# Kernel optimization log

Measured on AMD Instinct MI355X. Metric: run time of the kernel, lower is better.

## Reference

```python
import jax, jax.numpy as jnp
import numpy as np

CHUNK = 64
EMA_DECAY = 0.99


def setup_inputs() -> dict:
    key = jax.random.key(0)
    ks = jax.random.split(key, 4)
    Bsz, S, H, P, N = 2, 4096, 16, 64, 128
    X = jax.random.normal(ks[0], (Bsz, S, H, P), jnp.float32)
    # negative log-decay rates, as in Mamba-2 (A = -softplus(...) style)
    A = -jnp.abs(jax.random.normal(ks[1], (Bsz, S, H), jnp.float32)) * 0.1
    Bm = jax.random.normal(ks[2], (Bsz, S, H, N), jnp.float32) / np.sqrt(N)
    Cm = jax.random.normal(ks[3], (Bsz, S, H, N), jnp.float32) / np.sqrt(N)
    # ChunkedSurpriseGate parameters / buffers
    log2_alpha_base = jnp.full((H,), -0.15, jnp.float32)
    log2_beta = jnp.zeros((H,), jnp.float32)
    surprise_ema = jnp.ones((H,), jnp.float32)
    return {"X": X, "A": A, "Bm": Bm, "Cm": Cm,
            "log2_alpha_base": log2_alpha_base, "log2_beta": log2_beta,
            "surprise_ema": surprise_ema}


def _chunked_surprise_ssd(X, A, Bm, Cm, log2_alpha_base, log2_beta, surprise_ema):
    Bsz, S, H, P = X.shape
    N = Bm.shape[-1]
    cs = CHUNK
    nC = S // cs  # seqlen chosen divisible by chunk_size (no padding branch)

    # [B, nC, cs, H, ...] -> chunk-major [nC, B, H, cs, ...] for lax.scan
    Xc = X.reshape(Bsz, nC, cs, H, P).transpose(1, 0, 3, 2, 4)   # [nC,B,H,cs,P]
    Ac = A.reshape(Bsz, nC, cs, H).transpose(1, 0, 3, 2)          # [nC,B,H,cs]
    Bc = Bm.reshape(Bsz, nC, cs, H, N).transpose(1, 0, 3, 2, 4)   # [nC,B,H,cs,N]
    Cc = Cm.reshape(Bsz, nC, cs, H, N).transpose(1, 0, 3, 2, 4)   # [nC,B,H,cs,N]

    idx = jnp.arange(cs)
    tri = idx[:, None] >= idx[None, :]  # causal mask for decay matrix L

    # gate constants (per-head)
    alpha_base = 1.0 - jnp.exp2(jnp.clip(log2_alpha_base, -3.32, -0.015))  # [H]
    beta = jnp.exp2(jnp.clip(log2_beta, -2.0, 2.0))                         # [H]

    def step(carry, xs):
        h_prev, h_before, decay_prev, ema = carry
        c, X_c, A_c, B_c, C_c = xs
        first = c == 0

        # --- delayed state-based surprise: ||h_prev - decay_prev * h_before||^2
        err = jnp.mean((h_prev - decay_prev[..., None, None] * h_before) ** 2,
                       axis=(-2, -1))  # [B,H]
        # EMA update (training=True path; torch does it under no_grad)
        ema_new = jax.lax.stop_gradient(EMA_DECAY * ema + (1.0 - EMA_DECAY) * jnp.mean(err, axis=0))
        normalized = err / (ema_new[None, :] + 1e-6)                # [B,H]
        boost = jax.nn.relu(jnp.tanh(beta[None, :] * normalized))
        alpha = jnp.clip(alpha_base[None, :] + (1.0 - alpha_base[None, :]) * boost,
                         0.01, 0.999)
        # torch: decay_scale = (1-alpha).mean().item()  -> detached scalar
        ds = jax.lax.stop_gradient(jnp.mean(1.0 - alpha))
        decay_scale = jnp.where(first, jnp.float32(1.0), ds)
        ema_out = jnp.where(first, ema, ema_new)  # no gate call on chunk 0

        # --- single-chunk SSD ---
        Acs = jnp.cumsum(A_c * decay_scale, axis=-1)                 # [B,H,cs]
        # causal decay matrix L[i,j] = exp(Acs[i]-Acs[j]) for i>=j
        L = jnp.where(tri, jnp.exp(Acs[..., :, None] - Acs[..., None, :]), 0.0)
        CB = jnp.einsum('bhin,bhjn->bhij', C_c, B_c)
        Y_intra = jnp.einsum('bhij,bhjd->bhid', L * CB, X_c)
        decay_from_start = jnp.exp(Acs)                               # [B,H,cs]
        Y_inter = jnp.einsum('bhin,bhnd,bhi->bhid', C_c, h_prev, decay_from_start)
        decay_to_end = jnp.exp(Acs[..., -1:] - Acs)                   # [B,H,cs]
        h_contrib = jnp.einsum('bhtn,bhtd,bht->bhnd', B_c, X_c, decay_to_end)
        decay_total = jnp.exp(Acs[..., -1])                           # [B,H]
        h_end = decay_total[..., None, None] * h_prev + h_contrib

        return (h_end, h_prev, decay_total, ema_out), Y_intra + Y_inter

    h0 = jnp.zeros((Bsz, H, N, P), X.dtype)
    carry0 = (h0, h0, jnp.ones((Bsz, H), X.dtype), surprise_ema)
    xs = (jnp.arange(nC), Xc, Ac, Bc, Cc)
    _, Ys = jax.lax.scan(step, carry0, xs)  # [nC,B,H,cs,P]

    # stack dim=2, permute(0,2,3,1,4), reshape -> [B,S,H,P]
    Y = Ys.transpose(1, 0, 3, 2, 4).reshape(Bsz, S, H, P)
    return Y


def reference(X, A, Bm, Cm, log2_alpha_base, log2_beta, surprise_ema):
    return _chunked_surprise_ssd(X, A, Bm, Cm, log2_alpha_base, log2_beta, surprise_ema)
```

## Files before the change

### kernel.cpp

```cpp
#include <hip/hip_runtime.h>
#include <math.h>


#define CSZ 64
#define NCH 64
#define NHD 16
#define PD  64
#define ND  128
#define BHN 32
#define NTILES 2048
#define GGRID 64
#define SEQ 4096

#define WS_S   0
#define WS_EG  131072
#define WS_DS  262144
#define WS_HC  262400

using bf16x8 = __attribute__((ext_vector_type(8))) short;
using f32x4  = __attribute__((ext_vector_type(4))) float;

__device__ __forceinline__ short f2bf(float f) {
  union { float f; unsigned u; } v; v.f = f;
  unsigned r = (v.u + 0x7FFFu + ((v.u >> 16) & 1u)) >> 16;
  return (short)r;
}

__device__ __forceinline__ float bf2f(short s) {
  union { float f; unsigned u; } v;
  v.u = ((unsigned)(unsigned short)s) << 16;
  return v.f;
}

__device__ __forceinline__ void split4(float4 v, short4& hi, short4& lo) {
  hi.x = f2bf(v.x); lo.x = f2bf(v.x - bf2f(hi.x));
  hi.y = f2bf(v.y); lo.y = f2bf(v.y - bf2f(hi.y));
  hi.z = f2bf(v.z); lo.z = f2bf(v.z - bf2f(hi.z));
  hi.w = f2bf(v.w); lo.w = f2bf(v.w - bf2f(hi.w));
}

__global__ __launch_bounds__(256) void k_gramerr(
    const float* __restrict__ X, const float* __restrict__ A,
    const float* __restrict__ Bm, float* __restrict__ ws)
{
  __shared__ __align__(16) short BhiS[64*72];
  __shared__ __align__(16) short BloS[64*72];
  __shared__ __align__(16) short XhiS[64*72];
  __shared__ __align__(16) short XloS[64*72];
  __shared__ float Sl[CSZ];
  __shared__ float Zl[CSZ];
  short* Mhi = BhiS;
  short* Mlo = BloS;
  short* Uhi = XhiS;
  short* Ulo = XloS;

  const int tile = blockIdx.x;
  const int c  = tile & 63;
  const int bh = tile >> 6;
  const int b = bh >> 4, h = bh & 15;
  const int tid = threadIdx.x;

  const float* Bbase = Bm + ((size_t)(b*SEQ + c*CSZ)*NHD + h)*ND;
  const float* Xbase = X  + ((size_t)(b*SEQ + c*CSZ)*NHD + h)*PD;

  if (tid < CSZ) {
    float v = A[(size_t)(b*SEQ + c*CSZ + tid)*NHD + h];
    #pragma unroll
    for (int d = 1; d < 64; d <<= 1) {
      float n = __shfl_up(v, d);
      if (tid >= d) v += n;
    }
    Sl[tid] = v;
    ws[WS_S + tile*CSZ + tid] = v;
  }

  #pragma unroll
  for (int qq = 0; qq < 4; ++qq) {
    int lin = qq*256 + tid;
    int t = lin >> 4, c4 = (lin & 15)*4;
    float4 v = *(const float4*)(Bbase + (size_t)t*(NHD*ND) + c4);
    short4 hi, lo; split4(v, hi, lo);
    *(short4*)&BhiS[t*72 + c4] = hi;
    *(short4*)&BloS[t*72 + c4] = lo;
  }
  #pragma unroll
  for (int qq = 0; qq < 4; ++qq) {
    int lin = qq*256 + tid;
    int t = lin >> 4, p4 = (lin & 15)*4;
    float4 v = *(const float4*)(Xbase + (size_t)t*(NHD*PD) + p4);
    short4 hi, lo; split4(v, hi, lo);
    *(short4*)&XhiS[t*72 + p4] = hi;
    *(short4*)&XloS[t*72 + p4] = lo;
  }
  __syncthreads();

  if (tid < CSZ) Zl[tid] = Sl[63] - Sl[tid];

  const int w = tid >> 6;
  const int lane = tid & 63;
  const int m = lane & 15, q = lane >> 4;

  f32x4 z4 = {0.f,0.f,0.f,0.f};
  f32x4 gb[4], gx[4];
  #pragma unroll
  for (int i = 0; i < 4; ++i) { gb[i] = z4; gx[i] = z4; }

  #pragma unroll
  for (int kk = 0; kk < 2; ++kk) {
    const int ao = (w*16+m)*72 + kk*32 + q*8;
    bf16x8 ah = *(bf16x8*)&BhiS[ao];
    bf16x8 al = *(bf16x8*)&BloS[ao];
    #pragma unroll
    for (int ct = 0; ct < 4; ++ct) {
      const int bo = (ct*16+m)*72 + kk*32 + q*8;
      bf16x8 bhv = *(bf16x8*)&BhiS[bo];
      bf16x8 blv = *(bf16x8*)&BloS[bo];
      gb[ct] = __builtin_amdgcn_mfma_f32_16x16x32_bf16(ah, bhv, gb[ct], 0,0,0);
      gb[ct] = __builtin_amdgcn_mfma_f32_16x16x32_bf16(ah, blv, gb[ct], 0,0,0);
      gb[ct] = __builtin_amdgcn_mfma_f32_16x16x32_bf16(al, bhv, gb[ct], 0,0,0);
    }
  }
  __syncthreads();

  #pragma unroll
  for (int qq = 0; qq < 4; ++qq) {
    int lin = qq*256 + tid;
    int t = lin >> 4, c4 = (lin & 15)*4;
    float4 v = *(const float4*)(Bbase + (size_t)t*(NHD*ND) + 64 + c4);
    short4 hi, lo; split4(v, hi, lo);
    *(short4*)&BhiS[t*72 + c4] = hi;
    *(short4*)&BloS[t*72 + c4] = lo;
  }
  __syncthreads();

  #pragma unroll
  for (int kk = 0; kk < 2; ++kk) {
    const int ao = (w*16+m)*72 + kk*32 + q*8;
    bf16x8 ah = *(bf16x8*)&BhiS[ao];
    bf16x8 al = *(bf16x8*)&BloS[ao];
    #pragma unroll
    for (int ct = 0; ct < 4; ++ct) {
      const int bo = (ct*16+m)*72 + kk*32 + q*8;
      bf16x8 bhv = *(bf16x8*)&BhiS[bo];
      bf16x8 blv = *(bf16x8*)&BloS[bo];
      gb[ct] = __builtin_amdgcn_mfma_f32_16x16x32_bf16(ah, bhv, gb[ct], 0,0,0);
      gb[ct] = __builtin_amdgcn_mfma_f32_16x16x32_bf16(ah, blv, gb[ct], 0,0,0);
      gb[ct] = __builtin_amdgcn_mfma_f32_16x16x32_bf16(al, bhv, gb[ct], 0,0,0);
    }
  }
  #pragma unroll
  for (int kk = 0; kk < 2; ++kk) {
    const int ao = (w*16+m)*72 + kk*32 + q*8;
    bf16x8 ah = *(bf16x8*)&XhiS[ao];
    bf16x8 al = *(bf16x8*)&XloS[ao];
    #pragma unroll
    for (int ct = 0; ct < 4; ++ct) {
      const int bo = (ct*16+m)*72 + kk*32 + q*8;
      bf16x8 bhv = *(bf16x8*)&XhiS[bo];
      bf16x8 blv = *(bf16x8*)&XloS[bo];
      gx[ct] = __builtin_amdgcn_mfma_f32_16x16x32_bf16(ah, bhv, gx[ct], 0,0,0);
      gx[ct] = __builtin_amdgcn_mfma_f32_16x16x32_bf16(ah, blv, gx[ct], 0,0,0);
      gx[ct] = __builtin_amdgcn_mfma_f32_16x16x32_bf16(al, bhv, gx[ct], 0,0,0);
    }
  }
  __syncthreads();

  #pragma unroll
  for (int ct = 0; ct < 4; ++ct)
    #pragma unroll
    for (int r = 0; r < 4; ++r) {
      int i = w*16 + q*4 + r;
      int j = ct*16 + m;
      float mvf = gb[ct][r]*gx[ct][r]*(1.0f/8192.0f);
      short mh = f2bf(mvf);
      Mhi[i*72 + j] = mh;
      Mlo[i*72 + j] = f2bf(mvf - bf2f(mh));
    }
  #pragma unroll
  for (int qq = 0; qq < 16; ++qq) {
    int idx = qq*256 + tid;
    int g = idx >> 6, t = idx & 63;
    float u = expf(((float)g*(1.0f/63.0f))*Zl[t]);
    short uh = f2bf(u);
    Uhi[g*72 + t] = uh;
    Ulo[g*72 + t] = f2bf(u - bf2f(uh));
  }
  __syncthreads();

  f32x4 wv4[4];
  #pragma unroll
  for (int i = 0; i < 4; ++i) wv4[i] = z4;
  #pragma unroll
  for (int kk = 0; kk < 2; ++kk) {
    const int ao = (w*16+m)*72 + kk*32 + q*8;
    bf16x8 uh = *(bf16x8*)&Uhi[ao];
    bf16x8 ul = *(bf16x8*)&Ulo[ao];
    #pragma unroll
    for (int ct = 0; ct < 4; ++ct) {
      const int bo = (ct*16+m)*72 + kk*32 + q*8;
      bf16x8 mh = *(bf16x8*)&Mhi[bo];
      bf16x8 ml = *(bf16x8*)&Mlo[bo];
      wv4[ct] = __builtin_amdgcn_mfma_f32_16x16x32_bf16(uh, mh, wv4[ct], 0,0,0);
      wv4[ct] = __builtin_amdgcn_mfma_f32_16x16x32_bf16(uh, ml, wv4[ct], 0,0,0);
      wv4[ct] = __builtin_amdgcn_mfma_f32_16x16x32_bf16(ul, mh, wv4[ct], 0,0,0);
    }
  }

  #pragma unroll
  for (int r = 0; r < 4; ++r) {
    int g = w*16 + q*4 + r;
    float e = 0.f;
    #pragma unroll
    for (int ct = 0; ct < 4; ++ct) {
      int t = ct*16 + m;
      float uval = bf2f(Uhi[g*72 + t]) + bf2f(Ulo[g*72 + t]);
      e += wv4[ct][r] * uval;
    }
    e += __shfl_xor(e, 1);
    e += __shfl_xor(e, 2);
    e += __shfl_xor(e, 4);
    e += __shfl_xor(e, 8);
    if (m == 0) ws[WS_EG + (c*GGRID + g)*BHN + bh] = e;
  }
}

__global__ __launch_bounds__(64) void k_gate(
    const float* __restrict__ l2ab, const float* __restrict__ l2b,
    const float* __restrict__ sema, float* __restrict__ ws)
{
  __shared__ __align__(16) float ring[8*GGRID*BHN];
  const int lane = threadIdx.x;
  const int h = lane & 15;
  const float* EG = ws + WS_EG;

  float ab = 0.f, bt = 1.f, ema = 0.f;
  if (lane < NHD) {
    float la = fminf(fmaxf(l2ab[lane], -3.32f), -0.015f);
    ab = 1.0f - exp2f(la);
    float lb = fminf(fmaxf(l2b[lane], -2.0f), 2.0f);
    bt = exp2f(lb);
    ema = sema[lane];
  }
  const float ab_bh = __shfl(ab, h);
  const float bt_bh = __shfl(bt, h);

  #define ISSUE_SLAB(s)                                                        \
    {                                                                          \
      const float* gsrc = EG + (size_t)(s)*(GGRID*BHN) + lane*4;               \
      float* lbase = ring + ((s) & 7)*(GGRID*BHN);                             \
      _Pragma("unroll")                                                        \
      for (int r = 0; r < 8; ++r) {                                            \
        __builtin_amdgcn_global_load_lds(                                      \
            (const __attribute__((address_space(1))) void*)(gsrc + r*256),     \
            (__attribute__((address_space(3))) void*)(lbase + r*256),          \
            16, 0, 0);                                                         \
      }                                                                        \
    }

  #pragma unroll
  for (int s = 0; s < 6; ++s) ISSUE_SLAB(s);

  float ds_prev = 1.0f;
  if (lane == 0) ws[WS_DS + 0] = 1.0f;

  for (int c = 1; c < NCH; ++c) {
    const int j = c - 1;
    if (j + 6 <= 62) ISSUE_SLAB(j + 6);
    if (j <= 56) {
      asm volatile("s_waitcnt vmcnt(48)" ::: "memory");
    } else {
      asm volatile("s_waitcnt vmcnt(0)" ::: "memory");
    }
    __builtin_amdgcn_sched_barrier(0);
    const float* slab = ring + (j & 7)*(GGRID*BHN);

    float x = ds_prev * 63.0f;
    int ib = (int)floorf(x);
    ib = max(1, min(61, ib));
    float u = x - (float)ib;
    float err = 0.f;
    if (lane < BHN) {
      const float* p = slab + (ib-1)*BHN + lane;
      float ym1 = p[0], y0 = p[32], y1 = p[64], y2 = p[96];
      err = ym1*(u*(u-1.f)*(u-2.f))*(-1.f/6.f)
          + y0 *((u+1.f)*(u-1.f)*(u-2.f))*(0.5f)
          + y1 *((u+1.f)*u*(u-2.f))*(-0.5f)
          + y2 *((u+1.f)*u*(u-1.f))*(1.f/6.f);
    }
    float e0 = __shfl(err, h);
    float e1 = __shfl(err, 16 + h);
    float ema_new = 0.99f*ema + 0.01f*0.5f*(e0 + e1);
    float emv = __shfl(ema_new, h);
    float oma = 0.f;
    if (lane < BHN) {
      float normalized = err / (emv + 1e-6f);
      float boost = fmaxf(tanhf(bt_bh*normalized), 0.f);
      float alpha = ab_bh + (1.f - ab_bh)*boost;
      alpha = fminf(fmaxf(alpha, 0.01f), 0.999f);
      oma = 1.f - alpha;
    }
    float s = oma;
    s += __shfl_xor(s, 1);  s += __shfl_xor(s, 2);  s += __shfl_xor(s, 4);
    s += __shfl_xor(s, 8);  s += __shfl_xor(s, 16);
    float ds = __shfl(s, 0) * (1.0f/32.0f);
    if (lane < NHD) ema = ema_new;
    if (lane == 0) ws[WS_DS + c] = ds;
    ds_prev = ds;
  }
  #undef ISSUE_SLAB
}

__global__ __launch_bounds__(256, 4) void k_chunk(
    const float* __restrict__ X, const float* __restrict__ Bm,
    const float* __restrict__ Cm, float* __restrict__ ws,
    float* __restrict__ Y)
{
  __shared__ short Bs[64*72];
  __shared__ short BsTw[128*72];
  __shared__ short XsT[64*72];
  __shared__ float Acs[CSZ];
  __shared__ float Wl[CSZ];
  short* Es = Bs;

  const int tile = blockIdx.x;
  const int c  = tile & 63;
  const int bh = tile >> 6;
  const int b = bh >> 4, h = bh & 15;
  const int tid = threadIdx.x;
  const int w = tid >> 6;
  const int lane = tid & 63;
  const int m = lane & 15, q = lane >> 4;

  const float* Bbase = Bm + ((size_t)(b*SEQ + c*CSZ)*NHD + h)*ND;
  const float* Cbase = Cm + ((size_t)(b*SEQ + c*CSZ)*NHD + h)*ND;
  const float* Xbase = X  + ((size_t)(b*SEQ + c*CSZ)*NHD + h)*PD;

  const float* crow = Cbase + (size_t)(w*16 + m)*(NHD*ND);
  float4 cflo[4], cfhi[4];
  #pragma unroll
  for (int kk = 0; kk < 4; ++kk) {
    cflo[kk] = *(const float4*)(crow + kk*32 + q*8);
    cfhi[kk] = *(const float4*)(crow + kk*32 + q*8 + 4);
  }

  const float dsc = ws[WS_DS + c];
  if (tid < CSZ) {
    float sv  = ws[WS_S + tile*CSZ + tid];
    float s63 = ws[WS_S + tile*CSZ + 63];
    Acs[tid] = dsc*sv;
    Wl[tid]  = expf(dsc*(s63 - sv));
  }
  __syncthreads();

  #pragma unroll
  for (int qq = 0; qq < 4; ++qq) {
    int lin = qq*256 + tid;
    int t = lin >> 4, c4 = (lin & 15)*4;
    float4 bv = *(const float4*)(Bbase + (size_t)t*(NHD*ND) + c4);
    short4 bs4; bs4.x=f2bf(bv.x); bs4.y=f2bf(bv.y); bs4.z=f2bf(bv.z); bs4.w=f2bf(bv.w);
    *(short4*)&Bs[t*72 + c4] = bs4;
    float wt = Wl[t];
    BsTw[(c4+0)*72 + t] = f2bf(bv.x*wt);
    BsTw[(c4+1)*72 + t] = f2bf(bv.y*wt);
    BsTw[(c4+2)*72 + t] = f2bf(bv.z*wt);
    BsTw[(c4+3)*72 + t] = f2bf(bv.w*wt);
  }
  #pragma unroll
  for (int qq = 0; qq < 4; ++qq) {
    int lin = qq*256 + tid;
    int t = lin >> 4, p4 = (lin & 15)*4;
    float4 xv = *(const float4*)(Xbase + (size_t)t*(NHD*PD) + p4);
    XsT[(p4+0)*72 + t] = f2bf(xv.x);
    XsT[(p4+1)*72 + t] = f2bf(xv.y);
    XsT[(p4+2)*72 + t] = f2bf(xv.z);
    XsT[(p4+3)*72 + t] = f2bf(xv.w);
  }
  __syncthreads();

  bf16x8 af[4];
  #pragma unroll
  for (int kk = 0; kk < 4; ++kk) {
    bf16x8 t;
    t[0]=f2bf(cflo[kk].x); t[1]=f2bf(cflo[kk].y); t[2]=f2bf(cflo[kk].z); t[3]=f2bf(cflo[kk].w);
    t[4]=f2bf(cfhi[kk].x); t[5]=f2bf(cfhi[kk].y); t[6]=f2bf(cfhi[kk].z); t[7]=f2bf(cfhi[kk].w);
    af[kk] = t;
  }

  f32x4 acc0 = {0.f,0.f,0.f,0.f}, acc1 = acc0, acc2 = acc0, acc3 = acc0;
  #pragma unroll
  for (int kk = 0; kk < 2; ++kk) {
    bf16x8 b0 = *(bf16x8*)&Bs[( 0+m)*72 + kk*32 + q*8];
    bf16x8 b1 = *(bf16x8*)&Bs[(16+m)*72 + kk*32 + q*8];
    bf16x8 b2 = *(bf16x8*)&Bs[(32+m)*72 + kk*32 + q*8];
    bf16x8 b3 = *(bf16x8*)&Bs[(48+m)*72 + kk*32 + q*8];
    acc0 = __builtin_amdgcn_mfma_f32_16x16x32_bf16(af[kk], b0, acc0, 0,0,0);
    acc1 = __builtin_amdgcn_mfma_f32_16x16x32_bf16(af[kk], b1, acc1, 0,0,0);
    acc2 = __builtin_amdgcn_mfma_f32_16x16x32_bf16(af[kk], b2, acc2, 0,0,0);
    acc3 = __builtin_amdgcn_mfma_f32_16x16x32_bf16(af[kk], b3, acc3, 0,0,0);
  }
  __syncthreads();

  #pragma unroll
  for (int qq = 0; qq < 4; ++qq) {
    int lin = qq*256 + tid;
    int t = lin >> 4, c4 = (lin & 15)*4;
    float4 bv = *(const float4*)(Bbase + (size_t)t*(NHD*ND) + 64 + c4);
    short4 bs4; bs4.x=f2bf(bv.x); bs4.y=f2bf(bv.y); bs4.z=f2bf(bv.z); bs4.w=f2bf(bv.w);
    *(short4*)&Bs[t*72 + c4] = bs4;
    float wt = Wl[t];
    BsTw[(64+c4+0)*72 + t] = f2bf(bv.x*wt);
    BsTw[(64+c4+1)*72 + t] = f2bf(bv.y*wt);
    BsTw[(64+c4+2)*72 + t] = f2bf(bv.z*wt);
    BsTw[(64+c4+3)*72 + t] = f2bf(bv.w*wt);
  }
  __syncthreads();

  #pragma unroll
  for (int kk = 0; kk < 2; ++kk) {
    bf16x8 b0 = *(bf16x8*)&Bs[( 0+m)*72 + kk*32 + q*8];
    bf16x8 b1 = *(bf16x8*)&Bs[(16+m)*72 + kk*32 + q*8];
    bf16x8 b2 = *(bf16x8*)&Bs[(32+m)*72 + kk*32 + q*8];
    bf16x8 b3 = *(bf16x8*)&Bs[(48+m)*72 + kk*32 + q*8];
    acc0 = __builtin_amdgcn_mfma_f32_16x16x32_bf16(af[2+kk], b0, acc0, 0,0,0);
    acc1 = __builtin_amdgcn_mfma_f32_16x16x32_bf16(af[2+kk], b1, acc1, 0,0,0);
    acc2 = __builtin_amdgcn_mfma_f32_16x16x32_bf16(af[2+kk], b2, acc2, 0,0,0);
    acc3 = __builtin_amdgcn_mfma_f32_16x16x32_bf16(af[2+kk], b3, acc3, 0,0,0);
  }
  __syncthreads();

  {
    f32x4 accs[4] = {acc0, acc1, acc2, acc3};
    #pragma unroll
    for (int ct = 0; ct < 4; ++ct) {
      int j = ct*16 + m;
      float aj = Acs[j];
      #pragma unroll
      for (int r = 0; r < 4; ++r) {
        int i = w*16 + q*4 + r;
        float v = (i >= j) ? expf(Acs[i]-aj)*accs[ct][r] : 0.f;
        Es[i*72 + j] = f2bf(v);
      }
    }
  }

  f32x4 h00={0.f,0.f,0.f,0.f}, h01=h00, h02=h00, h03=h00;
  f32x4 h10=h00, h11=h00, h12=h00, h13=h00;
  #pragma unroll
  for (int kk = 0; kk < 2; ++kk) {
    bf16x8 a0 = *(bf16x8*)&BsTw[((2*w+0)*16+m)*72 + kk*32 + q*8];
    bf16x8 a1 = *(bf16x8*)&BsTw[((2*w+1)*16+m)*72 + kk*32 + q*8];
    bf16x8 x0 = *(bf16x8*)&XsT[( 0+m)*72 + kk*32 + q*8];
    bf16x8 x1 = *(bf16x8*)&XsT[(16+m)*72 + kk*32 + q*8];
    bf16x8 x2 = *(bf16x8*)&XsT[(32+m)*72 + kk*32 + q*8];
    bf16x8 x3 = *(bf16x8*)&XsT[(48+m)*72 + kk*32 + q*8];
    h00 = __builtin_amdgcn_mfma_f32_16x16x32_bf16(a0, x0, h00, 0,0,0);
    h01 = __builtin_amdgcn_mfma_f32_16x16x32_bf16(a0, x1, h01, 0,0,0);
    h02 = __builtin_amdgcn_mfma_f32_16x16x32_bf16(a0, x2, h02, 0,0,0);
    h03 = __builtin_amdgcn_mfma_f32_16x16x32_bf16(a0, x3, h03, 0,0,0);
    h10 = __builtin_amdgcn_mfma_f32_16x16x32_bf16(a1, x0, h10, 0,0,0);
    h11 = __builtin_amdgcn_mfma_f32_16x16x32_bf16(a1, x1, h11, 0,0,0);
    h12 = __builtin_amdgcn_mfma_f32_16x16x32_bf16(a1, x2, h12, 0,0,0);
    h13 = __builtin_amdgcn_mfma_f32_16x16x32_bf16(a1, x3, h13, 0,0,0);
  }

  f32x4 y0={0.f,0.f,0.f,0.f}, y1=y0, y2=y0, y3=y0;
  #pragma unroll
  for (int kk = 0; kk < 2; ++kk) {
    bf16x8 ef = *(bf16x8*)&Es[(w*16+m)*72 + kk*32 + q*8];
    bf16x8 x0 = *(bf16x8*)&XsT[( 0+m)*72 + kk*32 + q*8];
    bf16x8 x1 = *(bf16x8*)&XsT[(16+m)*72 + kk*32 + q*8];
    bf16x8 x2 = *(bf16x8*)&XsT[(32+m)*72 + kk*32 + q*8];
    bf16x8 x3 = *(bf16x8*)&XsT[(48+m)*72 + kk*32 + q*8];
    y0 = __builtin_amdgcn_mfma_f32_16x16x32_bf16(ef, x0, y0, 0,0,0);
    y1 = __builtin_amdgcn_mfma_f32_16x16x32_bf16(ef, x1, y1, 0,0,0);
    y2 = __builtin_amdgcn_mfma_f32_16x16x32_bf16(ef, x2, y2, 0,0,0);
    y3 = __builtin_amdgcn_mfma_f32_16x16x32_bf16(ef, x3, y3, 0,0,0);
  }

  {
    float* Ybase = Y + ((size_t)(b*SEQ + c*CSZ)*NHD + h)*PD;
    f32x4 ys[4] = {y0, y1, y2, y3};
    #pragma unroll
    for (int r = 0; r < 4; ++r) {
      int i = w*16 + q*4 + r;
      #pragma unroll
      for (int ct = 0; ct < 4; ++ct)
        Ybase[(size_t)i*(NHD*PD) + ct*16 + m] = ys[ct][r];
    }
  }
  {
    float* hcp = ws + WS_HC + (size_t)tile*(ND*PD);
    f32x4 hs[2][4] = {{h00,h01,h02,h03},{h10,h11,h12,h13}};
    #pragma unroll
    for (int nt = 0; nt < 2; ++nt)
      #pragma unroll
      for (int r = 0; r < 4; ++r) {
        int n = (2*w+nt)*16 + q*4 + r;
        #pragma unroll
        for (int pt = 0; pt < 4; ++pt)
          hcp[n*PD + pt*16 + m] = hs[nt][pt][r];
      }
  }
}

__global__ __launch_bounds__(256) void k_scan(float* __restrict__ ws)
{
  __shared__ float dtbl[NCH];
  const int bh = blockIdx.x >> 5, part = blockIdx.x & 31;
  const int tid = threadIdx.x;
  if (tid < NCH) {
    float s63 = ws[WS_S + (bh*NCH + tid)*CSZ + 63];
    dtbl[tid] = expf(ws[WS_DS + tid]*s63);
  }
  __syncthreads();
  float* base = ws + WS_HC + (size_t)bh*(NCH*ND*PD) + part*256 + tid;
  float hacc = 0.f;
  #pragma unroll 1
  for (int c = 0; c < NCH; ++c) {
    float* p = base + (size_t)c*(ND*PD);
    float v = *p;
    *p = hacc;
    hacc = dtbl[c]*hacc + v;
  }
}

__global__ __launch_bounds__(256, 4) void k_inter(
    const float* __restrict__ Cm, float* __restrict__ ws,
    float* __restrict__ Y)
{
  __shared__ short Cs[64*136];
  __shared__ short HsT[64*136];
  __shared__ float Dfs[CSZ];

  const int tile = blockIdx.x;
  const int c  = tile & 63;
  const int bh = tile >> 6;
  const int b = bh >> 4, h = bh & 15;
  const int tid = threadIdx.x;

  const float dsc = ws[WS_DS + c];
  if (tid < CSZ) Dfs[tid] = expf(dsc*ws[WS_S + tile*CSZ + tid]);

  const float* Cbase = Cm + ((size_t)(b*SEQ + c*CSZ)*NHD + h)*ND;
  const float* hp = ws + WS_HC + (size_t)tile*(ND*PD);
  #pragma unroll
  for (int qq = 0; qq < 8; ++qq) {
    int lin = qq*256 + tid;
    int t = lin >> 5, n4 = (lin & 31)*4;
    float4 cv = *(const float4*)(Cbase + (size_t)t*(NHD*ND) + n4);
    short4 cs4; cs4.x=f2bf(cv.x); cs4.y=f2bf(cv.y); cs4.z=f2bf(cv.z); cs4.w=f2bf(cv.w);
    *(short4*)&Cs[t*136 + n4] = cs4;
    int n = lin >> 4, p4 = (lin & 15)*4;
    float4 hv = *(const float4*)(hp + (size_t)lin*4);
    HsT[(p4+0)*136 + n] = f2bf(hv.x);
    HsT[(p4+1)*136 + n] = f2bf(hv.y);
    HsT[(p4+2)*136 + n] = f2bf(hv.z);
    HsT[(p4+3)*136 + n] = f2bf(hv.w);
  }
  __syncthreads();

  const int w = tid >> 6;
  const int lane = tid & 63;
  const int m = lane & 15, q = lane >> 4;

  f32x4 a0 = {0.f,0.f,0.f,0.f}, a1 = a0, a2 = a0, a3 = a0;
  #pragma unroll
  for (int kk = 0; kk < 4; ++kk) {
    bf16x8 cf = *(bf16x8*)&Cs[(w*16+m)*136 + kk*32 + q*8];
    bf16x8 hb0 = *(bf16x8*)&HsT[( 0+m)*136 + kk*32 + q*8];
    bf16x8 hb1 = *(bf16x8*)&HsT[(16+m)*136 + kk*32 + q*8];
    bf16x8 hb2 = *(bf16x8*)&HsT[(32+m)*136 + kk*32 + q*8];
    bf16x8 hb3 = *(bf16x8*)&HsT[(48+m)*136 + kk*32 + q*8];
    a0 = __builtin_amdgcn_mfma_f32_16x16x32_bf16(cf, hb0, a0, 0,0,0);
    a1 = __builtin_amdgcn_mfma_f32_16x16x32_bf16(cf, hb1, a1, 0,0,0);
    a2 = __builtin_amdgcn_mfma_f32_16x16x32_bf16(cf, hb2, a2, 0,0,0);
    a3 = __builtin_amdgcn_mfma_f32_16x16x32_bf16(cf, hb3, a3, 0,0,0);
  }

  float* Ybase = Y + ((size_t)(b*SEQ + c*CSZ)*NHD + h)*PD;
  f32x4 as[4] = {a0, a1, a2, a3};
  #pragma unroll
  for (int r = 0; r < 4; ++r) {
    int i = w*16 + q*4 + r;
    float d = Dfs[i];
    #pragma unroll
    for (int ct = 0; ct < 4; ++ct) {
      size_t idx = (size_t)i*(NHD*PD) + ct*16 + m;
      Ybase[idx] += d*as[ct][r];
    }
  }
}

extern "C" void kernel_launch(void* const* d_in, const int* in_sizes, int n_in,
                              void* d_out, int out_size, void* d_ws, size_t ws_size,
                              hipStream_t stream) {
  const float* X    = (const float*)d_in[0];
  const float* A    = (const float*)d_in[1];
  const float* Bm   = (const float*)d_in[2];
  const float* Cm   = (const float*)d_in[3];
  const float* l2ab = (const float*)d_in[4];
  const float* l2b  = (const float*)d_in[5];
  const float* sema = (const float*)d_in[6];
  float* Y  = (float*)d_out;
  float* ws = (float*)d_ws;

  hipLaunchKernelGGL(k_gramerr, dim3(NTILES), dim3(256), 0, stream, X, A, Bm, ws);
  hipLaunchKernelGGL(k_gate,    dim3(1),      dim3(64),  0, stream, l2ab, l2b, sema, ws);
  hipLaunchKernelGGL(k_chunk,   dim3(NTILES), dim3(256), 0, stream, X, Bm, Cm, ws, Y);
  hipLaunchKernelGGL(k_scan,    dim3(1024),   dim3(256), 0, stream, ws);
  hipLaunchKernelGGL(k_inter,   dim3(NTILES), dim3(256), 0, stream, Cm, ws, Y);
}
```

Baseline: 316.1 us.

## Fuse inter-chunk state scan into inter-chunk output kernel with register-held state

Replaces the separate k_scan and k_inter kernels with one k_scaninter kernel. Each 64-thread block owns one (b,h), a 16-column slice of P and a 16-row slice of each chunk. It keeps the running state in registers, prefetches the next chunk's contribution, and applies the C·h MFMA per chunk. This removes the in-place scan write-back, the reread of the full state array, and one launch. The cost is a serial 64-step loop over only 512 small blocks, so parallelism drops and each block redoes the state recurrence for its own slice.

```diff
diff --git a/kernel.cpp b/kernel.cpp
--- a/kernel.cpp
+++ b/kernel.cpp
@@ -503,92 +503,102 @@
   }
 }
 
-__global__ __launch_bounds__(256) void k_scan(float* __restrict__ ws)
-{
-  __shared__ float dtbl[NCH];
-  const int bh = blockIdx.x >> 5, part = blockIdx.x & 31;
-  const int tid = threadIdx.x;
-  if (tid < NCH) {
-    float s63 = ws[WS_S + (bh*NCH + tid)*CSZ + 63];
-    dtbl[tid] = expf(ws[WS_DS + tid]*s63);
-  }
-  __syncthreads();
-  float* base = ws + WS_HC + (size_t)bh*(NCH*ND*PD) + part*256 + tid;
-  float hacc = 0.f;
-  #pragma unroll 1
-  for (int c = 0; c < NCH; ++c) {
-    float* p = base + (size_t)c*(ND*PD);
-    float v = *p;
-    *p = hacc;
-    hacc = dtbl[c]*hacc + v;
-  }
-}
-
-__global__ __launch_bounds__(256, 4) void k_inter(
+__global__ __launch_bounds__(64) void k_scaninter(
     const float* __restrict__ Cm, float* __restrict__ ws,
     float* __restrict__ Y)
 {
-  __shared__ short Cs[64*136];
-  __shared__ short HsT[64*136];
-  __shared__ float Dfs[CSZ];
-
-  const int tile = blockIdx.x;
-  const int c  = tile & 63;
-  const int bh = tile >> 6;
+  const int blk = blockIdx.x;
+  const int bh = blk >> 4;
+  const int pp = (blk >> 2) & 3;
+  const int tt = blk & 3;
   const int b = bh >> 4, h = bh & 15;
-  const int tid = threadIdx.x;
-
-  const float dsc = ws[WS_DS + c];
-  if (tid < CSZ) Dfs[tid] = expf(dsc*ws[WS_S + tile*CSZ + tid]);
-
-  const float* Cbase = Cm + ((size_t)(b*SEQ + c*CSZ)*NHD + h)*ND;
-  const float* hp = ws + WS_HC + (size_t)tile*(ND*PD);
-  #pragma unroll
-  for (int qq = 0; qq < 8; ++qq) {
-    int lin = qq*256 + tid;
-    int t = lin >> 5, n4 = (lin & 31)*4;
-    float4 cv = *(const float4*)(Cbase + (size_t)t*(NHD*ND) + n4);
-    short4 cs4; cs4.x=f2bf(cv.x); cs4.y=f2bf(cv.y); cs4.z=f2bf(cv.z); cs4.w=f2bf(cv.w);
-    *(short4*)&Cs[t*136 + n4] = cs4;
-    int n = lin >> 4, p4 = (lin & 15)*4;
-    float4 hv = *(const float4*)(hp + (size_t)lin*4);
-    HsT[(p4+0)*136 + n] = f2bf(hv.x);
-    HsT[(p4+1)*136 + n] = f2bf(hv.y);
-    HsT[(p4+2)*136 + n] = f2bf(hv.z);
-    HsT[(p4+3)*136 + n] = f2bf(hv.w);
-  }
-  __syncthreads();
-
-  const int w = tid >> 6;
-  const int lane = tid & 63;
+  const int lane = threadIdx.x;
   const int m = lane & 15, q = lane >> 4;
-
-  f32x4 a0 = {0.f,0.f,0.f,0.f}, a1 = a0, a2 = a0, a3 = a0;
-  #pragma unroll
-  for (int kk = 0; kk < 4; ++kk) {
-    bf16x8 cf = *(bf16x8*)&Cs[(w*16+m)*136 + kk*32 + q*8];
-    bf16x8 hb0 = *(bf16x8*)&HsT[( 0+m)*136 + kk*32 + q*8];
-    bf16x8 hb1 = *(bf16x8*)&HsT[(16+m)*136 + kk*32 + q*8];
-    bf16x8 hb2 = *(bf16x8*)&HsT[(32+m)*136 + kk*32 + q*8];
-    bf16x8 hb3 = *(bf16x8*)&HsT[(48+m)*136 + kk*32 + q*8];
-    a0 = __builtin_amdgcn_mfma_f32_16x16x32_bf16(cf, hb0, a0, 0,0,0);
-    a1 = __builtin_amdgcn_mfma_f32_16x16x32_bf16(cf, hb1, a1, 0,0,0);
-    a2 = __builtin_amdgcn_mfma_f32_16x16x32_bf16(cf, hb2, a2, 0,0,0);
-    a3 = __builtin_amdgcn_mfma_f32_16x16x32_bf16(cf, hb3, a3, 0,0,0);
-  }
-
-  float* Ybase = Y + ((size_t)(b*SEQ + c*CSZ)*NHD + h)*PD;
-  f32x4 as[4] = {a0, a1, a2, a3};
-  #pragma unroll
-  for (int r = 0; r < 4; ++r) {
-    int i = w*16 + q*4 + r;
-    float d = Dfs[i];
-    #pragma unroll
-    for (int ct = 0; ct < 4; ++ct) {
-      size_t idx = (size_t)i*(NHD*PD) + ct*16 + m;
-      Ybase[idx] += d*as[ct][r];
-    }
-  }
+  const int p0 = pp*16;
+
+  float hreg[4][8];
+  #pragma unroll
+  for (int kk = 0; kk < 4; ++kk)
+    #pragma unroll
+    for (int i = 0; i < 8; ++i) hreg[kk][i] = 0.f;
+
+  float hcA[4][8], hcB[4][8];
+  {
+    const float* hc0 = ws + WS_HC + (size_t)(bh*NCH + 0)*(ND*PD);
+    #pragma unroll
+    for (int kk = 0; kk < 4; ++kk)
+      #pragma unroll
+      for (int i = 0; i < 8; ++i)
+        hcA[kk][i] = hc0[(size_t)(kk*32 + q*8 + i)*PD + p0 + m];
+  }
+
+  #define SI_STEP(CV, CUR, NXT)                                                \
+    {                                                                          \
+      const int c = (CV);                                                      \
+                         \
+      if (c + 1 < NCH) {                                                       \
+        const float* hcn = ws + WS_HC + (size_t)(bh*NCH + c + 1)*(ND*PD);      \
+        _Pragma("unroll")                                                      \
+        for (int kk = 0; kk < 4; ++kk)                                         \
+          _Pragma("unroll")                                                    \
+          for (int i = 0; i < 8; ++i)                                          \
+            NXT[kk][i] = hcn[(size_t)(kk*32 + q*8 + i)*PD + p0 + m];           \
+      }                                                                        \
+      const float dsc = ws[WS_DS + c];                                         \
+      const float* Sbase = ws + WS_S + (size_t)(bh*NCH + c)*CSZ;               \
+      const float dt = expf(dsc * Sbase[63]);                                  \
+      float dv = 0.f;                                                          \
+      if (lane < 16) dv = expf(dsc * Sbase[tt*16 + lane]);                     \
+                                   \
+      const float* Cb = Cm + ((size_t)(b*SEQ + c*CSZ)*NHD + h)*ND              \
+                         + (size_t)(tt*16 + m)*(NHD*ND);                       \
+      bf16x8 af[4];                                                            \
+      _Pragma("unroll")                                                        \
+      for (int kk = 0; kk < 4; ++kk) {                                         \
+        float4 lo = *(const float4*)(Cb + kk*32 + q*8);                        \
+        float4 hi = *(const float4*)(Cb + kk*32 + q*8 + 4);                    \
+        bf16x8 t;                                                              \
+        t[0]=f2bf(lo.x); t[1]=f2bf(lo.y); t[2]=f2bf(lo.z); t[3]=f2bf(lo.w);    \
+        t[4]=f2bf(hi.x); t[5]=f2bf(hi.y); t[6]=f2bf(hi.z); t[7]=f2bf(hi.w);    \
+        af[kk] = t;                                                            \
+      }                                                                        \
+                       \
+      bf16x8 hb[4];                                                            \
+      _Pragma("unroll")                                                        \
+      for (int kk = 0; kk < 4; ++kk) {                                         \
+        bf16x8 t;                                                              \
+        _Pragma("unroll")                                                      \
+        for (int i = 0; i < 8; ++i) t[i] = f2bf(hreg[kk][i]);                  \
+        hb[kk] = t;                                                            \
+      }                                                                        \
+      f32x4 acc = {0.f, 0.f, 0.f, 0.f};                                        \
+      acc = __builtin_amdgcn_mfma_f32_16x16x32_bf16(af[0], hb[0], acc, 0,0,0); \
+      acc = __builtin_amdgcn_mfma_f32_16x16x32_bf16(af[1], hb[1], acc, 0,0,0); \
+      acc = __builtin_amdgcn_mfma_f32_16x16x32_bf16(af[2], hb[2], acc, 0,0,0); \
+      acc = __builtin_amdgcn_mfma_f32_16x16x32_bf16(af[3], hb[3], acc, 0,0,0); \
+                                     \
+      float* Yb = Y + ((size_t)(b*SEQ + c*CSZ)*NHD + h)*PD;                    \
+      _Pragma("unroll")                                                        \
+      for (int r = 0; r < 4; ++r) {                                            \
+        int i = tt*16 + q*4 + r;                                               \
+        float d = __shfl(dv, q*4 + r);                                         \
+        size_t idx = (size_t)i*(NHD*PD) + p0 + m;                              \
+        Yb[idx] += d * acc[r];                                                 \
+      }                                                                        \
+                      \
+      _Pragma("unroll")                                                        \
+      for (int kk = 0; kk < 4; ++kk)                                           \
+        _Pragma("unroll")                                                      \
+        for (int i = 0; i < 8; ++i)                                            \
+          hreg[kk][i] = dt*hreg[kk][i] + CUR[kk][i];                           \
+    }
+
+  #pragma unroll 1
+  for (int cc = 0; cc < NCH; cc += 2) {
+    SI_STEP(cc,     hcA, hcB);
+    SI_STEP(cc + 1, hcB, hcA);
+  }
+  #undef SI_STEP
 }
 
 extern "C" void kernel_launch(void* const* d_in, const int* in_sizes, int n_in,
@@ -604,9 +614,8 @@
   float* Y  = (float*)d_out;
   float* ws = (float*)d_ws;
 
-  hipLaunchKernelGGL(k_gramerr, dim3(NTILES), dim3(256), 0, stream, X, A, Bm, ws);
-  hipLaunchKernelGGL(k_gate,    dim3(1),      dim3(64),  0, stream, l2ab, l2b, sema, ws);
-  hipLaunchKernelGGL(k_chunk,   dim3(NTILES), dim3(256), 0, stream, X, Bm, Cm, ws, Y);
-  hipLaunchKernelGGL(k_scan,    dim3(1024),   dim3(256), 0, stream, ws);
-  hipLaunchKernelGGL(k_inter,   dim3(NTILES), dim3(256), 0, stream, Cm, ws, Y);
-}
+  hipLaunchKernelGGL(k_gramerr,   dim3(NTILES), dim3(256), 0, stream, X, A, Bm, ws);
+  hipLaunchKernelGGL(k_gate,      dim3(1),      dim3(64),  0, stream, l2ab, l2b, sema, ws);
+  hipLaunchKernelGGL(k_chunk,     dim3(NTILES), dim3(256), 0, stream, X, Bm, Cm, ws, Y);
+  hipLaunchKernelGGL(k_scaninter, dim3(512),    dim3(64),  0, stream, Cm, ws, Y);
+}
```

Measured after the change: 417.1 us. 32.0% more time.
